# Kernel optimization log

Measured on AMD Instinct MI355X. Metric: run time of the kernel, lower is better.

The kernel has to match this reference:

```python
import jax, jax.numpy as jnp
import numpy as np

B, C_IN, C_OUT, H, W, W_DIM, K = 4, 64, 64, 512, 512, 512, 3
LRELU_SLOPE = 0.2
ACT_GAIN = np.sqrt(2.0).astype(np.float32)  # lrelu def_gain
CONV_CLAMP = 256.0


def setup_inputs() -> dict:
    key = jax.random.key(0)
    ks = jax.random.split(key, 5)
    return {
        "x": jax.random.normal(ks[0], (B, C_IN, H, W), dtype=jnp.float32),
        "ws": jax.random.normal(ks[1], (B, W_DIM), dtype=jnp.float32),
        "noise": jax.random.normal(ks[2], (B, 1, H, W), dtype=jnp.float32),
        "affine_weight": jax.random.normal(ks[3], (C_IN, W_DIM), dtype=jnp.float32),
        "affine_bias": jnp.ones((C_IN,), dtype=jnp.float32),
        "conv_weight": jax.random.normal(ks[4], (C_OUT, C_IN, K, K), dtype=jnp.float32),
        "bias": jnp.zeros((C_OUT,), dtype=jnp.float32),
    }


def reference(x, ws, noise, affine_weight, affine_bias, conv_weight, bias):
    b, c_in, h, w_sp = x.shape
    c_out, _, kh, kw = conv_weight.shape
    w_dim = ws.shape[1]

    # Affine (FullyConnectedLayer with equalized LR: weight_gain = 1/sqrt(w_dim), bias_init=1)
    styles = ws @ (affine_weight.T * np.float32(1.0 / np.sqrt(w_dim))) + affine_bias  # [b, c_in]

    # Modulate per-sample weights: w = weight[None] * styles
    wmod = conv_weight[None] * styles[:, None, :, None, None]  # [b, c_out, c_in, kh, kw]

    # Demodulation coefficients
    demod = jax.lax.rsqrt(jnp.sum(jnp.square(wmod), axis=(2, 3, 4)) + 1e-8)  # [b, c_out]
    wmod = wmod * demod[:, :, None, None, None]

    # Fused grouped conv: groups = batch (conv2d_resample, up=down=1, flip_weight=True -> correlation)
    xg = x.reshape(1, b * c_in, h, w_sp)
    wg = wmod.reshape(b * c_out, c_in, kh, kw)
    pad = kh // 2
    y = jax.lax.conv_general_dilated(
        xg, wg, window_strides=(1, 1), padding=[(pad, pad), (pad, pad)],
        dimension_numbers=("NCHW", "OIHW", "NCHW"), feature_group_count=b)
    y = y.reshape(b, c_out, h, w_sp)

    # Noise add (broadcast over channels)
    y = y + noise

    # bias_act: bias + lrelu * act_gain, then clamp (conv_clamp * gain, gain=1)
    y = y + bias[None, :, None, None]
    y = jnp.where(y >= 0, y, LRELU_SLOPE * y) * ACT_GAIN
    y = jnp.clip(y, -CONV_CLAMP, CONV_CLAMP)
    return y
```

## Files before the change

kernel.cpp:

```cpp
#include <hip/hip_runtime.h>
#include <math.h>

#define HH 512
#define WW 512
#define HW (HH * WW)
#define PW 514
#define PPIX (PW * PW)

#define A_U 36864
#define B_U 22016
#define LDS_BYTES ((A_U + 2 * B_U) * 2)

typedef short bf16x8 __attribute__((ext_vector_type(8)));
typedef float f32x4  __attribute__((ext_vector_type(4)));
typedef float f32x16 __attribute__((ext_vector_type(16)));

__device__ __forceinline__ ushort f2bf(float f) {
    union { float f; uint u; } c; c.f = f;
    uint u = c.u;
    return (ushort)((u + 0x7fffu + ((u >> 16) & 1u)) >> 16);
}

__device__ __forceinline__ uint cvtpk(float a, float b) {
    uint r;
    asm("v_cvt_pk_bf16_f32 %0, %1, %2" : "=v"(r) : "v"(a), "v"(b));
    return r;
}

__global__ void k_styles(const float* __restrict__ wsv, const float* __restrict__ aw,
                         const float* __restrict__ ab, float* __restrict__ styles) {
    int bid = blockIdx.x;
    int b = bid >> 6, ci = bid & 63;
    int l = threadIdx.x;
    const float* wrow = wsv + b * 512;
    const float* arow = aw + ci * 512;
    float s = 0.f;
    #pragma unroll
    for (int j = 0; j < 8; ++j)
        s += wrow[l + 64 * j] * arow[l + 64 * j];
    #pragma unroll
    for (int off = 32; off; off >>= 1)
        s += __shfl_xor(s, off, 64);
    if (l == 0)
        styles[b * 64 + ci] = s * 0.044194173824159216f + ab[ci];
}

__global__ void k_wmod(const float* __restrict__ cw, const float* __restrict__ styles,
                       ushort* __restrict__ wb) {
    int b = blockIdx.x >> 6, co = blockIdx.x & 63;
    int ci = threadIdx.x;
    float st = styles[b * 64 + ci];
    const float* wp = cw + (co * 64 + ci) * 9;
    float wv[9];
    float ss = 0.f;
    #pragma unroll
    for (int k = 0; k < 9; ++k) { wv[k] = wp[k] * st; ss += wv[k] * wv[k]; }
    #pragma unroll
    for (int off = 32; off; off >>= 1)
        ss += __shfl_xor(ss, off, 64);
    float dm = 1.0f / sqrtf(ss + 1e-8f);
    int cisw = ((((ci >> 3) ^ co) & 7) << 3) | (ci & 7);
    #pragma unroll
    for (int k = 0; k < 9; ++k)
        wb[((size_t)(b * 64 + co) * 9 + k) * 64 + cisw] = f2bf(wv[k] * dm);
}

__global__ __launch_bounds__(256) void k_xpose(
    const float* __restrict__ x, ushort* __restrict__ xp) {
    const int t = threadIdx.x;
    const int bid = blockIdx.x;

    if (bid >= 8192) {
        int id = (bid - 8192) * 256 + t;
        if (id >= 4 * 2052) return;
        int b = id / 2052, r = id % 2052;
        int gyp, gxp;
        if (r < 514)       { gyp = 0;        gxp = r; }
        else if (r < 1028) { gyp = 513;      gxp = r - 514; }
        else if (r < 1540) { gyp = r - 1027; gxp = 0; }
        else               { gyp = r - 1539; gxp = 513; }
        ushort* p = xp + (((size_t)b * PW + gyp) * PW + gxp) * 64;
        uint4 z = make_uint4(0, 0, 0, 0);
        #pragma unroll
        for (int i = 0; i < 8; ++i) *(uint4*)(p + i * 8) = z;
        return;
    }

    __shared__ ushort lt[128 * 68];
    const int gxt = bid & 3;
    const int gy  = (bid >> 2) & 511;
    const int b   = bid >> 11;

    const float* xb = x + (size_t)b * 64 * HW + (size_t)gy * WW + gxt * 128;
    const int ci0 = 8 * (t >> 5);
    const int gxc = t & 31;

    f32x4 v[8];
    #pragma unroll
    for (int j = 0; j < 8; ++j)
        v[j] = *(const f32x4*)(xb + (size_t)(ci0 + j) * HW + gxc * 4);

    #pragma unroll
    for (int p = 0; p < 4; ++p) {
        int px = gxc * 4 + p;
        int rowp = ((px & 3) * 32 + (px >> 2)) * 68;
        #pragma unroll
        for (int cg = 0; cg < 2; ++cg) {
            uint lo = cvtpk(v[4 * cg + 0][p], v[4 * cg + 1][p]);
            uint hi = cvtpk(v[4 * cg + 2][p], v[4 * cg + 3][p]);
            *(uint2*)&lt[rowp + ci0 + 4 * cg] = make_uint2(lo, hi);
        }
    }
    __syncthreads();

    const int px = t >> 1, half = t & 1;
    const int rowp = ((px & 3) * 32 + (px >> 2)) * 68 + half * 32;
    uint4 o0 = *(uint4*)&lt[rowp + 0];
    uint4 o1 = *(uint4*)&lt[rowp + 8];
    uint4 o2 = *(uint4*)&lt[rowp + 16];
    uint4 o3 = *(uint4*)&lt[rowp + 24];
    ushort* dst = xp + (((size_t)b * PW + (gy + 1)) * PW + (gxt * 128 + px + 1)) * 64
                     + half * 32;
    *(uint4*)(dst + 0)  = o0;
    *(uint4*)(dst + 8)  = o1;
    *(uint4*)(dst + 16) = o2;
    *(uint4*)(dst + 24) = o3;
}

__global__ __launch_bounds__(256, 1) void k_conv(
    const ushort* __restrict__ xp,
    const ushort* __restrict__ wb,
    const float* __restrict__ noise,
    const float* __restrict__ bias,
    float* __restrict__ out) {
    extern __shared__ __align__(16) ushort lds[];

    const int t = threadIdx.x;
    const int w = t >> 6;
    const int lane = t & 63;
    const int n5 = lane & 31;
    const int hl = lane >> 5;
    const int blk = blockIdx.x;
    const int b = blk >> 6;
    const int band = blk & 63;
    const int ty = band * 8;

    const ushort* xpb = xp + (size_t)b * PPIX * 64;
    const ushort* wA  = wb + (size_t)b * 64 * 576;

    #pragma unroll
    for (int jj = 0; jj < 18; ++jj) {
        int j = w + jj * 4;
        const ushort* src = wA + j * 512 + lane * 8;
        __builtin_amdgcn_global_load_lds(
            (const __attribute__((address_space(1))) unsigned int*)src,
            (__attribute__((address_space(3))) unsigned int*)&lds[j * 512],
            16, 0, 0);
    }

    int soff[11];
    #pragma unroll
    for (int jj = 0; jj < 11; ++jj) {
        int j = w + jj * 4;
        if (j < 43) {
            int c = j * 64 + lane;
            int c2 = c < 2719 ? c : 2719;
            int cig = c2 & 7;
            int pxl = c2 >> 3;
            int row = pxl / 34;
            int lcol = pxl - row * 34;
            int gsrc = cig ^ (lcol & 7);
            soff[jj] = ((ty + row) * PW + lcol) * 64 + gsrc * 8;
        } else soff[jj] = 0;
    }

    #pragma unroll
    for (int jj = 0; jj < 11; ++jj) {
        int j = w + jj * 4;
        if (j < 43)
            __builtin_amdgcn_global_load_lds(
                (const __attribute__((address_space(1))) unsigned int*)(xpb + soff[jj]),
                (__attribute__((address_space(3))) unsigned int*)&lds[A_U + j * 512],
                16, 0, 0);
    }
    asm volatile("s_waitcnt vmcnt(0)" ::: "memory");
    __syncthreads();

    int aidx[2];
    #pragma unroll
    for (int mt = 0; mt < 2; ++mt)
        aidx[mt] = (mt * 32 + n5) * 576 + ((hl ^ (n5 & 7)) << 3);

    int bidx[2][3];
    const int brow = 2 * w + (n5 >> 4);
    #pragma unroll
    for (int i = 0; i < 2; ++i)
        #pragma unroll
        for (int dx = 0; dx < 3; ++dx) {
            int lcol = i * 16 + (n5 & 15) + dx;
            bidx[i][dx] = (brow * 34 + lcol) * 64 + ((hl ^ (lcol & 7)) << 3);
        }

    const float* nz = noise + (size_t)b * HW;
    const int orow = ty + brow;

    int p = 0;
    for (int it = 0; it < 16; ++it) {
        const int tx = it * 32;

        float nv[2];
        #pragma unroll
        for (int i = 0; i < 2; ++i)
            nv[i] = nz[orow * WW + tx + i * 16 + (n5 & 15)];

        if (it < 15) {
            #pragma unroll
            for (int jj = 0; jj < 11; ++jj) {
                int j = w + jj * 4;
                if (j < 43)
                    __builtin_amdgcn_global_load_lds(
                        (const __attribute__((address_space(1))) unsigned int*)
                            (xpb + soff[jj] + (tx + 32) * 64),
                        (__attribute__((address_space(3))) unsigned int*)
                            &lds[A_U + (p ^ 1) * B_U + j * 512],
                        16, 0, 0);
            }
        }

        const ushort* bufp = &lds[A_U + p * B_U];
        f32x16 acc[2][2];
        #pragma unroll
        for (int mt = 0; mt < 2; ++mt)
            #pragma unroll
            for (int i = 0; i < 2; ++i)
                acc[mt][i] = (f32x16){0.f,0.f,0.f,0.f,0.f,0.f,0.f,0.f,
                                      0.f,0.f,0.f,0.f,0.f,0.f,0.f,0.f};

        #pragma unroll
        for (int dy = 0; dy < 3; ++dy) {
            #pragma unroll
            for (int dx = 0; dx < 3; ++dx) {
                const int off = dy * 3 + dx;
                #pragma unroll
                for (int kb = 0; kb < 4; ++kb) {
                    bf16x8 afr[2], bfr[2];
                    #pragma unroll
                    for (int mt = 0; mt < 2; ++mt)
                        afr[mt] = *(const bf16x8*)
                            &lds[(aidx[mt] + off * 64) ^ (kb << 4)];
                    #pragma unroll
                    for (int i = 0; i < 2; ++i)
                        bfr[i] = *(const bf16x8*)
                            &bufp[(bidx[i][dx] + dy * (34 * 64)) ^ (kb << 4)];
                    #pragma unroll
                    for (int mt = 0; mt < 2; ++mt)
                        #pragma unroll
                        for (int i = 0; i < 2; ++i)
                            acc[mt][i] = __builtin_amdgcn_mfma_f32_32x32x16_bf16(
                                afr[mt], bfr[i], acc[mt][i], 0, 0, 0);
                }
            }
        }

        #pragma unroll
        for (int mt = 0; mt < 2; ++mt) {
            #pragma unroll
            for (int i = 0; i < 2; ++i) {
                const int ocol = tx + i * 16 + (n5 & 15);
                #pragma unroll
                for (int reg = 0; reg < 16; ++reg) {
                    int co = mt * 32 + (reg & 3) + 8 * (reg >> 2) + 4 * hl;
                    float y = acc[mt][i][reg] + nv[i] + bias[co];
                    y = (y >= 0.f ? y : 0.2f * y) * 1.41421356237f;
                    y = fminf(fmaxf(y, -256.f), 256.f);
                    out[((size_t)(b * 64 + co) * HH + orow) * WW + ocol] = y;
                }
            }
        }

        asm volatile("s_waitcnt vmcnt(63)" ::: "memory");
        __builtin_amdgcn_sched_barrier(0);
        __builtin_amdgcn_s_barrier();
        p ^= 1;
    }
}

extern "C" void kernel_launch(void* const* d_in, const int* in_sizes, int n_in,
                              void* d_out, int out_size, void* d_ws, size_t ws_size,
                              hipStream_t stream) {
    const float* x     = (const float*)d_in[0];
    const float* wsv   = (const float*)d_in[1];
    const float* noise = (const float*)d_in[2];
    const float* aw    = (const float*)d_in[3];
    const float* ab    = (const float*)d_in[4];
    const float* cw    = (const float*)d_in[5];
    const float* bias  = (const float*)d_in[6];
    float* out = (float*)d_out;

    float*  styles = (float*)d_ws;
    ushort* wb16   = (ushort*)((char*)d_ws + 1024);
    ushort* xpad   = (ushort*)((char*)d_ws + (1 << 20));

    hipFuncSetAttribute((const void*)k_conv,
                        hipFuncAttributeMaxDynamicSharedMemorySize, LDS_BYTES);

    k_styles<<<256, 64, 0, stream>>>(wsv, aw, ab, styles);
    k_wmod<<<256, 64, 0, stream>>>(cw, styles, wb16);
    k_xpose<<<8225, 256, 0, stream>>>(x, xpad);
    k_conv<<<256, 256, LDS_BYTES, stream>>>(xpad, wb16, noise, bias, out);
}
```

Measured before the change: 231.8 us.

## Split conv output channels across eight waves per block

The conv kernel goes from 256 to 512 threads per block. Each wave now computes one 32-channel half of the output instead of both halves. Weight and input tile loads are spread over eight waves, and the vmcnt wait threshold drops to match the smaller per-thread load and store count. The aim is more waves in flight to hide LDS, global load and output store latency, at the cost of loading the B fragments twice (once per channel half) from LDS.

```diff
diff --git a/kernel.cpp b/kernel.cpp
--- a/kernel.cpp
+++ b/kernel.cpp
@@ -127,7 +127,7 @@
     *(uint4*)(dst + 24) = o3;
 }
 
-__global__ __launch_bounds__(256, 1) void k_conv(
+__global__ __launch_bounds__(512, 1) void k_conv(
     const ushort* __restrict__ xp,
     const ushort* __restrict__ wb,
     const float* __restrict__ noise,
@@ -140,6 +140,8 @@
     const int lane = t & 63;
     const int n5 = lane & 31;
     const int hl = lane >> 5;
+    const int mtw = w >> 2;
+    const int rp  = w & 3;
     const int blk = blockIdx.x;
     const int b = blk >> 6;
     const int band = blk & 63;
@@ -149,8 +151,8 @@
     const ushort* wA  = wb + (size_t)b * 64 * 576;
 
     #pragma unroll
-    for (int jj = 0; jj < 18; ++jj) {
-        int j = w + jj * 4;
+    for (int jj = 0; jj < 9; ++jj) {
+        int j = w + jj * 8;
         const ushort* src = wA + j * 512 + lane * 8;
         __builtin_amdgcn_global_load_lds(
             (const __attribute__((address_space(1))) unsigned int*)src,
@@ -158,10 +160,10 @@
             16, 0, 0);
     }
 
-    int soff[11];
-    #pragma unroll
-    for (int jj = 0; jj < 11; ++jj) {
-        int j = w + jj * 4;
+    int soff[6];
+    #pragma unroll
+    for (int jj = 0; jj < 6; ++jj) {
+        int j = w + jj * 8;
         if (j < 43) {
             int c = j * 64 + lane;
             int c2 = c < 2719 ? c : 2719;
@@ -175,8 +177,8 @@
     }
 
     #pragma unroll
-    for (int jj = 0; jj < 11; ++jj) {
-        int j = w + jj * 4;
+    for (int jj = 0; jj < 6; ++jj) {
+        int j = w + jj * 8;
         if (j < 43)
             __builtin_amdgcn_global_load_lds(
                 (const __attribute__((address_space(1))) unsigned int*)(xpb + soff[jj]),
@@ -186,13 +188,10 @@
     asm volatile("s_waitcnt vmcnt(0)" ::: "memory");
     __syncthreads();
 
-    int aidx[2];
-    #pragma unroll
-    for (int mt = 0; mt < 2; ++mt)
-        aidx[mt] = (mt * 32 + n5) * 576 + ((hl ^ (n5 & 7)) << 3);
+    const int aidx = (mtw * 32 + n5) * 576 + ((hl ^ (n5 & 7)) << 3);
 
     int bidx[2][3];
-    const int brow = 2 * w + (n5 >> 4);
+    const int brow = 2 * rp + (n5 >> 4);
     #pragma unroll
     for (int i = 0; i < 2; ++i)
         #pragma unroll
@@ -215,8 +214,8 @@
 
         if (it < 15) {
             #pragma unroll
-            for (int jj = 0; jj < 11; ++jj) {
-                int j = w + jj * 4;
+            for (int jj = 0; jj < 6; ++jj) {
+                int j = w + jj * 8;
                 if (j < 43)
                     __builtin_amdgcn_global_load_lds(
                         (const __attribute__((address_space(1))) unsigned int*)
@@ -228,13 +227,11 @@
         }
 
         const ushort* bufp = &lds[A_U + p * B_U];
-        f32x16 acc[2][2];
-        #pragma unroll
-        for (int mt = 0; mt < 2; ++mt)
-            #pragma unroll
-            for (int i = 0; i < 2; ++i)
-                acc[mt][i] = (f32x16){0.f,0.f,0.f,0.f,0.f,0.f,0.f,0.f,
-                                      0.f,0.f,0.f,0.f,0.f,0.f,0.f,0.f};
+        f32x16 acc[2];
+        #pragma unroll
+        for (int i = 0; i < 2; ++i)
+            acc[i] = (f32x16){0.f,0.f,0.f,0.f,0.f,0.f,0.f,0.f,
+                              0.f,0.f,0.f,0.f,0.f,0.f,0.f,0.f};
 
         #pragma unroll
         for (int dy = 0; dy < 3; ++dy) {
@@ -243,42 +240,34 @@
                 const int off = dy * 3 + dx;
                 #pragma unroll
                 for (int kb = 0; kb < 4; ++kb) {
-                    bf16x8 afr[2], bfr[2];
-                    #pragma unroll
-                    for (int mt = 0; mt < 2; ++mt)
-                        afr[mt] = *(const bf16x8*)
-                            &lds[(aidx[mt] + off * 64) ^ (kb << 4)];
+                    bf16x8 afr, bfr[2];
+                    afr = *(const bf16x8*)&lds[(aidx + off * 64) ^ (kb << 4)];
                     #pragma unroll
                     for (int i = 0; i < 2; ++i)
                         bfr[i] = *(const bf16x8*)
                             &bufp[(bidx[i][dx] + dy * (34 * 64)) ^ (kb << 4)];
                     #pragma unroll
-                    for (int mt = 0; mt < 2; ++mt)
-                        #pragma unroll
-                        for (int i = 0; i < 2; ++i)
-                            acc[mt][i] = __builtin_amdgcn_mfma_f32_32x32x16_bf16(
-                                afr[mt], bfr[i], acc[mt][i], 0, 0, 0);
+                    for (int i = 0; i < 2; ++i)
+                        acc[i] = __builtin_amdgcn_mfma_f32_32x32x16_bf16(
+                            afr, bfr[i], acc[i], 0, 0, 0);
                 }
             }
         }
 
         #pragma unroll
-        for (int mt = 0; mt < 2; ++mt) {
+        for (int i = 0; i < 2; ++i) {
+            const int ocol = tx + i * 16 + (n5 & 15);
             #pragma unroll
-            for (int i = 0; i < 2; ++i) {
-                const int ocol = tx + i * 16 + (n5 & 15);
-                #pragma unroll
-                for (int reg = 0; reg < 16; ++reg) {
-                    int co = mt * 32 + (reg & 3) + 8 * (reg >> 2) + 4 * hl;
-                    float y = acc[mt][i][reg] + nv[i] + bias[co];
-                    y = (y >= 0.f ? y : 0.2f * y) * 1.41421356237f;
-                    y = fminf(fmaxf(y, -256.f), 256.f);
-                    out[((size_t)(b * 64 + co) * HH + orow) * WW + ocol] = y;
-                }
+            for (int reg = 0; reg < 16; ++reg) {
+                int co = mtw * 32 + (reg & 3) + 8 * (reg >> 2) + 4 * hl;
+                float y = acc[i][reg] + nv[i] + bias[co];
+                y = (y >= 0.f ? y : 0.2f * y) * 1.41421356237f;
+                y = fminf(fmaxf(y, -256.f), 256.f);
+                out[((size_t)(b * 64 + co) * HH + orow) * WW + ocol] = y;
             }
         }
 
-        asm volatile("s_waitcnt vmcnt(63)" ::: "memory");
+        asm volatile("s_waitcnt vmcnt(32)" ::: "memory");
         __builtin_amdgcn_sched_barrier(0);
         __builtin_amdgcn_s_barrier();
         p ^= 1;
@@ -307,5 +296,5 @@
     k_styles<<<256, 64, 0, stream>>>(wsv, aw, ab, styles);
     k_wmod<<<256, 64, 0, stream>>>(cw, styles, wb16);
     k_xpose<<<8225, 256, 0, stream>>>(x, xpad);
-    k_conv<<<256, 256, LDS_BYTES, stream>>>(xpad, wb16, noise, bias, out);
-}
+    k_conv<<<256, 512, LDS_BYTES, stream>>>(xpad, wb16, noise, bias, out);
+}
```

Result: no change. 234.7 us (+1.2%).
